# Kernel optimization log

Measured on AMD Instinct MI355X. Metric: run time of the kernel, lower is better.

Reference implementation:

```python
import jax, jax.numpy as jnp
import numpy as np
import math

B_SZ, T, D_IN, D_OUT, N = 8, 4096, 128, 128, 256
MAX_PHASE, RMIN, RMAX = math.pi, 0.0, 1.0


def setup_inputs() -> dict:
    key = jax.random.key(0)
    ks = jax.random.split(key, 9)
    x = jax.random.normal(ks[0], (B_SZ, T, D_IN), dtype=jnp.float32)
    # lambda parameterization exactly as in LRU.__init__
    u1 = jax.random.uniform(ks[1], (N,), minval=1e-4, maxval=1.0)
    u2 = jax.random.uniform(ks[2], (N,), minval=1e-4, maxval=1.0)
    nu_log = jnp.log(-0.5 * jnp.log(u1 * (RMAX + RMIN) * (RMAX - RMIN) + RMIN ** 2))
    theta_log = jnp.log(MAX_PHASE * u2)
    lam_abs = jnp.exp(-jnp.exp(nu_log))
    gamma_log = jnp.log(jnp.sqrt(1.0 - jnp.square(lam_abs)))
    B_re = jax.random.normal(ks[3], (N, D_IN)) / math.sqrt(2 * D_IN)
    B_im = jax.random.normal(ks[4], (N, D_IN)) / math.sqrt(2 * D_IN)
    C_re = jax.random.normal(ks[5], (D_OUT, N)) / math.sqrt(N)
    C_im = jax.random.normal(ks[6], (D_OUT, N)) / math.sqrt(N)
    D = jax.random.normal(ks[7], (D_OUT, D_IN)) / math.sqrt(D_IN)
    return {"x": x, "nu_log": nu_log, "theta_log": theta_log, "gamma_log": gamma_log,
            "B_re": B_re, "B_im": B_im, "C_re": C_re, "C_im": C_im, "D": D}


def _binary_op_diag(e1, e2):
    a1, b1 = e1
    a2, b2 = e2
    return a1 * a2, a2 * b1 + b2


def reference(x, nu_log, theta_log, gamma_log, B_re, B_im, C_re, C_im, D):
    # ss_params()
    lam_abs = jnp.exp(-jnp.exp(nu_log))
    phase = jnp.exp(theta_log)
    lam = (lam_abs * jnp.cos(phase) + 1j * (lam_abs * jnp.sin(phase))).astype(jnp.complex64)  # [N]
    gammas = jnp.exp(gamma_log)[:, None]
    Bc = (gammas * (B_re + 1j * B_im)).astype(jnp.complex64)  # [N, D_IN]
    Cc = (C_re + 1j * C_im).astype(jnp.complex64)             # [D_OUT, N]
    # diagonal complex linear recurrence via associative scan over time
    Bu = x.astype(Bc.dtype) @ Bc.T                            # [B, T, N] complex
    lam_el = jnp.broadcast_to(lam, Bu.shape)                  # [B, T, N]
    _, states = jax.lax.associative_scan(_binary_op_diag, (lam_el, Bu), axis=1)
    y = jnp.real(states @ Cc.T) + x @ D.T                     # [B, T, D_OUT]
    return y
```

## Files before the change

kernel.cpp:

```cpp
#include <hip/hip_runtime.h>
#include <math.h>

#define B_SZ 8
#define T_LEN 4096
#define D_IN 128
#define D_OUT 128
#define N_ST 256
#define BT (B_SZ * T_LEN)
#define CHUNK 64
#define NCHUNK (T_LEN / CHUNK)
#define NBLK (B_SZ * NCHUNK)

typedef __attribute__((ext_vector_type(8))) short short8;
typedef __attribute__((ext_vector_type(4))) float f32x4;
typedef unsigned int uint;
typedef unsigned short ushort;

static __device__ __forceinline__ short f2bf(float f) {
  union { float f; uint u; } v; v.f = f;
  uint r = v.u + 0x7FFFu + ((v.u >> 16) & 1u);
  return (short)(r >> 16);
}
static __device__ __forceinline__ float bf2f(uint h) {
  union { uint u; float f; } v; v.u = h << 16;
  return v.f;
}
static __device__ __forceinline__ uint pack2(float a, float b) {
  return (uint)(ushort)f2bf(a) | ((uint)(ushort)f2bf(b) << 16);
}

__global__ __launch_bounds__(256) void k0_setup(
    const float* __restrict__ x,
    const float* __restrict__ nu_log, const float* __restrict__ theta_log,
    const float* __restrict__ gamma_log,
    const float* __restrict__ B_re, const float* __restrict__ B_im,
    const float* __restrict__ C_re, const float* __restrict__ C_im,
    const float* __restrict__ Dm,
    short* __restrict__ Wf1, short* __restrict__ Wf2,
    float2* __restrict__ lampow2, short* __restrict__ xbf) {
  int blk = blockIdx.x;
  if (blk < 320) {
    int idx = blk * 256 + threadIdx.x;
    if (idx < 16 * 512 * 8) {
      int j = idx & 7, col = (idx >> 3) & 511, kg = idx >> 12;
      int k = kg * 8 + j;
      int n = col >> 1, ri = col & 1;
      float g = expf(gamma_log[n]);
      float v = g * (ri ? B_im[n * D_IN + k] : B_re[n * D_IN + k]);
      Wf1[idx] = f2bf(v);
    }
    if (idx < 80 * 128 * 8) {
      int j = idx & 7, d = (idx >> 3) & 127, kg = idx >> 10;
      int k = kg * 8 + j;
      float v;
      if (k < 512) {
        int n = k >> 1;
        v = (k & 1) ? -C_im[d * N_ST + n] : C_re[d * N_ST + n];
      } else {
        v = Dm[d * D_IN + (k - 512)];
      }
      Wf2[idx] = f2bf(v);
    }
  } else if (blk < 385) {
    int j = blk - 320;
    int n = threadIdx.x;
    float e_nu = expf(nu_log[n]);
    float phase = expf(theta_log[n]);
    float r = expf(-(float)j * e_nu);
    float a = (float)j * phase;
    float2 v; v.x = r * cosf(a); v.y = r * sinf(a);
    lampow2[j * N_ST + n] = v;
  } else {
    size_t i = (size_t)(blk - 385) * 256 + threadIdx.x;
    const float4* x4 = (const float4*)x;
    float4 a = x4[2 * i], b = x4[2 * i + 1];
    uint4 u;
    u.x = pack2(a.x, a.y); u.y = pack2(a.z, a.w);
    u.z = pack2(b.x, b.y); u.w = pack2(b.z, b.w);
    ((uint4*)xbf)[i] = u;
  }
}

__global__ __launch_bounds__(256, 2) void kA(
    const short* __restrict__ xbf, const short* __restrict__ Wf1,
    const float2* __restrict__ lampow2, float2* __restrict__ E) {
  __shared__ short bu[64 * 520];

  int bc = blockIdx.x;
  size_t row0 = (size_t)bc * CHUNK;
  int tid = threadIdx.x;
  int lane = tid & 63, w = tid >> 6;
  int m = lane & 15, q = lane >> 4;

  f32x4 acc[32];
#pragma unroll
  for (int ct = 0; ct < 32; ++ct) acc[ct] = (f32x4){0.f, 0.f, 0.f, 0.f};

  const short* xrow = xbf + (row0 + 16 * w + m) * D_IN;

  for (int ks = 0; ks < 4; ++ks) {
    short8 af = *(const short8*)(xrow + 32 * ks + 8 * q);
    const short* wbase = Wf1 + ((size_t)(4 * ks + q) * 512 + m) * 8;
#pragma unroll
    for (int ct = 0; ct < 32; ++ct) {
      short8 bf = *(const short8*)(wbase + 16 * ct * 8);
      acc[ct] = __builtin_amdgcn_mfma_f32_16x16x32_bf16(af, bf, acc[ct], 0, 0, 0);
    }
  }

#pragma unroll
  for (int ct = 0; ct < 32; ++ct) {
#pragma unroll
    for (int r = 0; r < 4; ++r) {
      bu[(16 * w + 4 * q + r) * 520 + 16 * ct + m] = f2bf(acc[ct][r]);
    }
  }
  __syncthreads();

  int n = tid;
  float2 lam = lampow2[N_ST + n];
  float sre = 0.f, sim = 0.f;
  for (int j = 0; j < CHUNK; ++j) {
    uint p = ((const uint*)(bu + j * 520))[n];
    float br = bf2f(p & 0xffffu), bi = bf2f(p >> 16);
    float nr = fmaf(lam.x, sre, fmaf(-lam.y, sim, br));
    float ni = fmaf(lam.x, sim, fmaf(lam.y, sre, bi));
    sre = nr; sim = ni;
  }
  float2 e; e.x = sre; e.y = sim;
  E[bc * N_ST + n] = e;
}

__global__ __launch_bounds__(256) void kB(
    const float2* __restrict__ E, const float2* __restrict__ lampow2,
    float2* __restrict__ P) {
  __shared__ float2 Es[NCHUNK * N_ST];

  int b = blockIdx.x;
  int tid = threadIdx.x;

  const float4* src = (const float4*)(E + (size_t)b * NCHUNK * N_ST);
  float4* dst = (float4*)Es;
#pragma unroll
  for (int it = 0; it < (NCHUNK * N_ST / 2) / 256; ++it) {
    dst[it * 256 + tid] = src[it * 256 + tid];
  }
  __syncthreads();

  int n = tid;
  float2 lamL = lampow2[CHUNK * N_ST + n];
  float cre = 0.f, cim = 0.f;
  for (int c = 0; c < NCHUNK; ++c) {
    size_t i = ((size_t)b * NCHUNK + c) * N_ST + n;
    float2 pv; pv.x = cre; pv.y = cim;
    P[i] = pv;
    float2 e = Es[c * N_ST + n];
    float nre = fmaf(lamL.x, cre, fmaf(-lamL.y, cim, e.x));
    float nim = fmaf(lamL.x, cim, fmaf(lamL.y, cre, e.y));
    cre = nre; cim = nim;
  }
}

__global__ __launch_bounds__(256, 1) void kC(
    const short* __restrict__ xbf, const short* __restrict__ Wf1,
    const float2* __restrict__ P, const float2* __restrict__ lampow2,
    const short* __restrict__ Wf2, float* __restrict__ y) {
  __shared__ short bu[64 * 520];
  __shared__ short As[64 * 640];

  int bc = blockIdx.x;
  size_t row0 = (size_t)bc * CHUNK;
  int tid = threadIdx.x;
  int lane = tid & 63, w = tid >> 6;
  int m = lane & 15, q = lane >> 4;

  f32x4 acc[32];
#pragma unroll
  for (int ct = 0; ct < 32; ++ct) acc[ct] = (f32x4){0.f, 0.f, 0.f, 0.f};

  const short* xrow = xbf + (row0 + 16 * w + m) * D_IN;

  for (int ks = 0; ks < 4; ++ks) {
    short8 af = *(const short8*)(xrow + 32 * ks + 8 * q);
    const short* wbase = Wf1 + ((size_t)(4 * ks + q) * 512 + m) * 8;
#pragma unroll
    for (int ct = 0; ct < 32; ++ct) {
      short8 bf = *(const short8*)(wbase + 16 * ct * 8);
      acc[ct] = __builtin_amdgcn_mfma_f32_16x16x32_bf16(af, bf, acc[ct], 0, 0, 0);
    }
  }

#pragma unroll
  for (int ct = 0; ct < 32; ++ct) {
#pragma unroll
    for (int r = 0; r < 4; ++r) {
      bu[(16 * w + 4 * q + r) * 520 + 16 * ct + m] = f2bf(acc[ct][r]);
    }
  }

  {
    int kxp = tid & 63, r0 = tid >> 6;
    int k = 512 + 2 * kxp;
    int g = k >> 3, koff = k & 7;
    for (int rr = 0; rr < 16; ++rr) {
      int row = r0 * 16 + rr;
      uint xv = *(const uint*)(xbf + (row0 + row) * D_IN + 2 * kxp);
      int gp = (g & ~7) | ((g + row) & 7);
      *(uint*)(As + row * 640 + gp * 8 + koff) = xv;
    }
  }
  __syncthreads();

  {
    int n = tid;
    float2 lam = lampow2[N_ST + n];
    float2 pc = P[(size_t)bc * N_ST + n];
    float sre = 0.f, sim = 0.f;
    int g2 = n >> 2, koff2 = (2 * n) & 7;
    for (int j = 0; j < CHUNK; ++j) {
      uint p = ((const uint*)(bu + j * 520))[n];
      float br = bf2f(p & 0xffffu), bi = bf2f(p >> 16);
      float nr = fmaf(lam.x, sre, fmaf(-lam.y, sim, br));
      float ni = fmaf(lam.x, sim, fmaf(lam.y, sre, bi));
      sre = nr; sim = ni;
      uint sp = pack2(sre, sim);
      float2 lp = lampow2[(size_t)(j + 1) * N_ST + n];
      float sr = bf2f(sp & 0xffffu) + lp.x * pc.x - lp.y * pc.y;
      float si = bf2f(sp >> 16)     + lp.x * pc.y + lp.y * pc.x;
      int gp = (g2 & ~7) | ((g2 + j) & 7);
      *(uint*)(As + j * 640 + gp * 8 + koff2) = pack2(sr, si);
    }
  }
  __syncthreads();

  int rw = w & 1, ch = w >> 1;

  f32x4 acc2[2][4];
#pragma unroll
  for (int rt = 0; rt < 2; ++rt)
#pragma unroll
    for (int ci = 0; ci < 4; ++ci) acc2[rt][ci] = (f32x4){0.f, 0.f, 0.f, 0.f};

  for (int ks = 0; ks < 20; ++ks) {
    int g = 4 * ks + q;
    int arow0 = 32 * rw + m;
    int gp = (g & ~7) | ((g + arow0) & 7);
    short8 af0 = *(const short8*)(As + arow0 * 640 + gp * 8);
    short8 af1 = *(const short8*)(As + (arow0 + 16) * 640 + gp * 8);
    const short* wbase = Wf2 + ((size_t)g * 128 + m) * 8;
#pragma unroll
    for (int ci = 0; ci < 4; ++ci) {
      int ctg = 4 * ch + ci;
      short8 bf = *(const short8*)(wbase + 16 * ctg * 8);
      acc2[0][ci] = __builtin_amdgcn_mfma_f32_16x16x32_bf16(af0, bf, acc2[0][ci], 0, 0, 0);
      acc2[1][ci] = __builtin_amdgcn_mfma_f32_16x16x32_bf16(af1, bf, acc2[1][ci], 0, 0, 0);
    }
  }

#pragma unroll
  for (int ci = 0; ci < 4; ++ci) {
    int ctg = 4 * ch + ci;
#pragma unroll
    for (int rt = 0; rt < 2; ++rt) {
#pragma unroll
      for (int r = 0; r < 4; ++r) {
        y[(row0 + 32 * rw + 16 * rt + 4 * q + r) * D_OUT + 16 * ctg + m] = acc2[rt][ci][r];
      }
    }
  }
}

extern "C" void kernel_launch(void* const* d_in, const int* in_sizes, int n_in,
                              void* d_out, int out_size, void* d_ws, size_t ws_size,
                              hipStream_t stream) {
  const float* x         = (const float*)d_in[0];
  const float* nu_log    = (const float*)d_in[1];
  const float* theta_log = (const float*)d_in[2];
  const float* gamma_log = (const float*)d_in[3];
  const float* B_re      = (const float*)d_in[4];
  const float* B_im      = (const float*)d_in[5];
  const float* C_re      = (const float*)d_in[6];
  const float* C_im      = (const float*)d_in[7];
  const float* Dm        = (const float*)d_in[8];
  float* y = (float*)d_out;

  char* wp = (char*)d_ws;
  float2* lampow2 = (float2*)wp; wp += (size_t)(CHUNK + 1) * N_ST * sizeof(float2);
  short*  Wf1     = (short*)wp;  wp += (size_t)16 * 512 * 8 * sizeof(short);
  short*  Wf2     = (short*)wp;  wp += (size_t)80 * 128 * 8 * sizeof(short);
  float2* E       = (float2*)wp; wp += (size_t)NBLK * N_ST * sizeof(float2);
  float2* P       = (float2*)wp; wp += (size_t)NBLK * N_ST * sizeof(float2);
  short*  xbf     = (short*)wp;  wp += (size_t)BT * D_IN * sizeof(short);

  hipLaunchKernelGGL(k0_setup, dim3(385 + BT * D_IN / 8 / 256), dim3(256), 0, stream,
                     x, nu_log, theta_log, gamma_log, B_re, B_im, C_re, C_im,
                     Dm, Wf1, Wf2, lampow2, xbf);
  hipLaunchKernelGGL(kA, dim3(NBLK), dim3(256), 0, stream,
                     xbf, Wf1, lampow2, E);
  hipLaunchKernelGGL(kB, dim3(B_SZ), dim3(256), 0, stream,
                     E, lampow2, P);
  hipLaunchKernelGGL(kC, dim3(NBLK), dim3(256), 0, stream,
                     xbf, Wf1, P, lampow2, Wf2, y);
}
```

Before: 157.1 us.

## Drop second LDS tile in kC, reuse bu buffer and load x fragments directly

Removes the 80KB As shared buffer so kC uses only the bu buffer (~66KB), and raises launch bounds to allow two blocks per CU. The scan now writes bf16 states back into bu in place, then a separate vectorized pass adds the carried-in prefix term lambda^(j+1)*P. The D-projection x operand is loaded from global memory straight into registers instead of being staged in LDS. In exchange it adds an extra barrier and pass over LDS, and the 2-wave occupancy target may force register spills given the 32 accumulator tiles.

```diff
diff --git a/kernel.cpp b/kernel.cpp
--- a/kernel.cpp
+++ b/kernel.cpp
@@ -161,12 +161,11 @@
   }
 }
 
-__global__ __launch_bounds__(256, 1) void kC(
+__global__ __launch_bounds__(256, 2) void kC(
     const short* __restrict__ xbf, const short* __restrict__ Wf1,
     const float2* __restrict__ P, const float2* __restrict__ lampow2,
     const short* __restrict__ Wf2, float* __restrict__ y) {
   __shared__ short bu[64 * 520];
-  __shared__ short As[64 * 640];
 
   int bc = blockIdx.x;
   size_t row0 = (size_t)bc * CHUNK;
@@ -197,43 +196,69 @@
       bu[(16 * w + 4 * q + r) * 520 + 16 * ct + m] = f2bf(acc[ct][r]);
     }
   }
-
-  {
-    int kxp = tid & 63, r0 = tid >> 6;
-    int k = 512 + 2 * kxp;
-    int g = k >> 3, koff = k & 7;
-    for (int rr = 0; rr < 16; ++rr) {
-      int row = r0 * 16 + rr;
-      uint xv = *(const uint*)(xbf + (row0 + row) * D_IN + 2 * kxp);
-      int gp = (g & ~7) | ((g + row) & 7);
-      *(uint*)(As + row * 640 + gp * 8 + koff) = xv;
-    }
-  }
   __syncthreads();
 
   {
     int n = tid;
     float2 lam = lampow2[N_ST + n];
-    float2 pc = P[(size_t)bc * N_ST + n];
     float sre = 0.f, sim = 0.f;
-    int g2 = n >> 2, koff2 = (2 * n) & 7;
     for (int j = 0; j < CHUNK; ++j) {
       uint p = ((const uint*)(bu + j * 520))[n];
       float br = bf2f(p & 0xffffu), bi = bf2f(p >> 16);
       float nr = fmaf(lam.x, sre, fmaf(-lam.y, sim, br));
       float ni = fmaf(lam.x, sim, fmaf(lam.y, sre, bi));
       sre = nr; sim = ni;
-      uint sp = pack2(sre, sim);
-      float2 lp = lampow2[(size_t)(j + 1) * N_ST + n];
-      float sr = bf2f(sp & 0xffffu) + lp.x * pc.x - lp.y * pc.y;
-      float si = bf2f(sp >> 16)     + lp.x * pc.y + lp.y * pc.x;
-      int gp = (g2 & ~7) | ((g2 + j) & 7);
-      *(uint*)(As + j * 640 + gp * 8 + koff2) = pack2(sr, si);
+      ((uint*)(bu + j * 520))[n] = pack2(sre, sim);
+    }
+  }
+  __syncthreads();
+
+  {
+    int n4 = tid & 63, rblk = tid >> 6;
+    float4 pA = *(const float4*)(P + (size_t)bc * N_ST + 4 * n4);
+    float4 pB = *(const float4*)(P + (size_t)bc * N_ST + 4 * n4 + 2);
+#pragma unroll
+    for (int rr = 0; rr < 16; ++rr) {
+      int row = rblk * 16 + rr;
+      uint4 sp = *(const uint4*)(bu + row * 520 + 8 * n4);
+      float4 lpa = *(const float4*)(lampow2 + ((size_t)(row + 1) * N_ST + 4 * n4));
+      float4 lpb = *(const float4*)(lampow2 + ((size_t)(row + 1) * N_ST + 4 * n4 + 2));
+      uint4 outv;
+      {
+        float sr = bf2f(sp.x & 0xffffu) + lpa.x * pA.x - lpa.y * pA.y;
+        float si = bf2f(sp.x >> 16)     + lpa.x * pA.y + lpa.y * pA.x;
+        outv.x = pack2(sr, si);
+      }
+      {
+        float sr = bf2f(sp.y & 0xffffu) + lpa.z * pA.z - lpa.w * pA.w;
+        float si = bf2f(sp.y >> 16)     + lpa.z * pA.w + lpa.w * pA.z;
+        outv.y = pack2(sr, si);
+      }
+      {
+        float sr = bf2f(sp.z & 0xffffu) + lpb.x * pB.x - lpb.y * pB.y;
+        float si = bf2f(sp.z >> 16)     + lpb.x * pB.y + lpb.y * pB.x;
+        outv.z = pack2(sr, si);
+      }
+      {
+        float sr = bf2f(sp.w & 0xffffu) + lpb.z * pB.z - lpb.w * pB.w;
+        float si = bf2f(sp.w >> 16)     + lpb.z * pB.w + lpb.w * pB.z;
+        outv.w = pack2(sr, si);
+      }
+      *(uint4*)(bu + row * 520 + 8 * n4) = outv;
     }
   }
   __syncthreads();
 
   int rw = w & 1, ch = w >> 1;
+  int arow0 = 32 * rw + m;
+
+  short8 xa0[4], xa1[4];
+#pragma unroll
+  for (int t = 0; t < 4; ++t) {
+    int g = 64 + 4 * t + q;
+    xa0[t] = *(const short8*)(xbf + (row0 + arow0) * D_IN + (g - 64) * 8);
+    xa1[t] = *(const short8*)(xbf + (row0 + arow0 + 16) * D_IN + (g - 64) * 8);
+  }
 
   f32x4 acc2[2][4];
 #pragma unroll
@@ -241,12 +266,10 @@
 #pragma unroll
     for (int ci = 0; ci < 4; ++ci) acc2[rt][ci] = (f32x4){0.f, 0.f, 0.f, 0.f};
 
-  for (int ks = 0; ks < 20; ++ks) {
+  for (int ks = 0; ks < 16; ++ks) {
     int g = 4 * ks + q;
-    int arow0 = 32 * rw + m;
-    int gp = (g & ~7) | ((g + arow0) & 7);
-    short8 af0 = *(const short8*)(As + arow0 * 640 + gp * 8);
-    short8 af1 = *(const short8*)(As + (arow0 + 16) * 640 + gp * 8);
+    short8 af0 = *(const short8*)(bu + arow0 * 520 + 8 * g);
+    short8 af1 = *(const short8*)(bu + (arow0 + 16) * 520 + 8 * g);
     const short* wbase = Wf2 + ((size_t)g * 128 + m) * 8;
 #pragma unroll
     for (int ci = 0; ci < 4; ++ci) {
@@ -254,6 +277,18 @@
       short8 bf = *(const short8*)(wbase + 16 * ctg * 8);
       acc2[0][ci] = __builtin_amdgcn_mfma_f32_16x16x32_bf16(af0, bf, acc2[0][ci], 0, 0, 0);
       acc2[1][ci] = __builtin_amdgcn_mfma_f32_16x16x32_bf16(af1, bf, acc2[1][ci], 0, 0, 0);
+    }
+  }
+#pragma unroll
+  for (int t = 0; t < 4; ++t) {
+    int g = 64 + 4 * t + q;
+    const short* wbase = Wf2 + ((size_t)g * 128 + m) * 8;
+#pragma unroll
+    for (int ci = 0; ci < 4; ++ci) {
+      int ctg = 4 * ch + ci;
+      short8 bf = *(const short8*)(wbase + 16 * ctg * 8);
+      acc2[0][ci] = __builtin_amdgcn_mfma_f32_16x16x32_bf16(xa0[t], bf, acc2[0][ci], 0, 0, 0);
+      acc2[1][ci] = __builtin_amdgcn_mfma_f32_16x16x32_bf16(xa1[t], bf, acc2[1][ci], 0, 0, 0);
     }
   }
 
```

Measured after the change: 140.2 us. 10.8% less time.
